# Optimization experiments

Measured on AMD Instinct MI355X. Metric: run time of the kernel, lower is better.

## Reference

```python
import jax, jax.numpy as jnp
import numpy as np

B, N, E = 128, 16384, 1048576
H, C = 512, 10


def setup_inputs() -> dict:
    key = jax.random.key(0)
    ks = jax.random.split(key, 10)
    x = jax.random.normal(ks[0], (B, N), dtype=jnp.float32)
    edge_index = jax.random.randint(ks[1], (2, E), 0, N, dtype=jnp.int64)
    edge_weight = jax.random.uniform(ks[2], (E,), dtype=jnp.float32)
    W1 = jax.random.normal(ks[3], (H, N), dtype=jnp.float32) * (1.0 / np.sqrt(N))
    b1 = jax.random.normal(ks[4], (H,), dtype=jnp.float32) * 0.01
    W2 = jax.random.normal(ks[5], (H, H), dtype=jnp.float32) * (1.0 / np.sqrt(H))
    b2 = jax.random.normal(ks[6], (H,), dtype=jnp.float32) * 0.01
    Wfc = jax.random.normal(ks[7], (C, H), dtype=jnp.float32) * (1.0 / np.sqrt(H))
    bfc = jax.random.normal(ks[8], (C,), dtype=jnp.float32) * 0.01
    return {"x": x, "edge_index": edge_index, "edge_weight": edge_weight,
            "W1": W1, "b1": b1, "W2": W2, "b2": b2, "Wfc": Wfc, "bfc": bfc}


def _sgconv_propagate(x, edge_index, edge_weight):
    """One GCN-normalized propagation (SGConv K=1, lin.weight==1, no bias).
    Batched edge offsets in the original == same operator applied per row.
    x: (B, N); edge_index: (2, E); edge_weight: (E,). Returns (B, N).
    """
    n = x.shape[1]
    src, dst = edge_index[0], edge_index[1]
    loop = jnp.arange(n, dtype=src.dtype)
    src_f = jnp.concatenate([src, loop])
    dst_f = jnp.concatenate([dst, loop])
    w_f = jnp.concatenate([edge_weight, jnp.ones((n,), x.dtype)])  # self-loop weight 1
    deg = jax.ops.segment_sum(w_f, dst_f, num_segments=n)  # in-degree (col)
    dinv = jnp.where(deg > 0, jax.lax.rsqrt(jnp.maximum(deg, 1e-12)), 0.0)
    norm = dinv[src_f] * w_f * dinv[dst_f]  # (E+N,)
    msgs = x[:, src_f] * norm  # (B, E+N) gather + scale
    return jax.ops.segment_sum(msgs.T, dst_f, num_segments=n).T  # scatter-add -> (B, N)


def reference(x, edge_index, edge_weight, W1, b1, W2, b2, Wfc, bfc):
    h = _sgconv_propagate(x, edge_index, edge_weight)  # diffusion (B, N)
    h = jax.nn.relu(h @ W1.T + b1)  # Linear(N->H) + ReLU
    h = jax.nn.relu(h @ W2.T + b2)  # Linear(H->H) + ReLU
    return h @ Wfc.T + bfc  # fc (H->C), softmax=False, dropout=0 (eval)
```

## Files before the change

kernel.cpp:

```cpp
#include <hip/hip_runtime.h>
#include <hip/hip_bf16.h>
#include <stdint.h>

#define B_DIM 128
#define N_DIM 16384
#define E_DIM 1048576
#define H_DIM 512
#define C_DIM 10
#define NWG 256
#define CHUNK (E_DIM / NWG)
#define NWORD8 (N_DIM / 4)
#define NGRP 8
#define WPG (NWG / NGRP)
#define SPLITK 64
#define KC (N_DIM / SPLITK)
#define WMASK 0xFFFFC000u
#define SMASK 0x3FFFu

typedef __attribute__((ext_vector_type(8))) short short8;
typedef __attribute__((ext_vector_type(4))) float f32x4;

__device__ __forceinline__ uint32_t f2bf(float f) {
    uint32_t u = __float_as_uint(f);
    return (u + 0x7fffu + ((u >> 16) & 1u)) >> 16;
}

__device__ __forceinline__ uint32_t encE(int s, float w) {
    uint32_t wb = __float_as_uint(w);
    return ((wb + 0x2000u) & WMASK) | (uint32_t)s;
}

__global__ void __launch_bounds__(256) k_hist1(const int* __restrict__ dst,
                                               uint32_t* __restrict__ slab) {
    __shared__ uint32_t ls[NWORD8];
    int bid = blockIdx.x, t = threadIdx.x;
#pragma unroll
    for (int i = 0; i < NWORD8 / 256; i++) ls[i * 256 + t] = 0;
    __syncthreads();
#pragma unroll
    for (int i = 0; i < CHUNK / 1024; i++) {
        int4 d4 = *(const int4*)&dst[bid * CHUNK + i * 1024 + t * 4];
        atomicAdd(&ls[d4.x >> 2], 1u << ((d4.x & 3) << 3));
        atomicAdd(&ls[d4.y >> 2], 1u << ((d4.y & 3) << 3));
        atomicAdd(&ls[d4.z >> 2], 1u << ((d4.z & 3) << 3));
        atomicAdd(&ls[d4.w >> 2], 1u << ((d4.w & 3) << 3));
    }
    __syncthreads();
#pragma unroll
    for (int i = 0; i < NWORD8 / 256; i++)
        slab[(size_t)bid * NWORD8 + i * 256 + t] = ls[i * 256 + t];
}

__global__ void __launch_bounds__(128) k_scanA8(uint32_t* __restrict__ slab,
                                                uint32_t* __restrict__ grp) {
    int b = blockIdx.x;
    int g = b >> 5;
    int j = (b & 31) * 128 + threadIdx.x;
    uint32_t run = 0;
    for (int w = g * WPG; w < (g + 1) * WPG; w++) {
        uint32_t c = slab[(size_t)w * NWORD8 + j];
        slab[(size_t)w * NWORD8 + j] = run;
        run += c;
    }
    grp[(size_t)g * NWORD8 + j] = run;
}

__global__ void __launch_bounds__(1024) k_scanBC8(uint32_t* __restrict__ grp,
                                                  int* __restrict__ offs) {
    __shared__ uint32_t part[1024];
    int t = threadIdx.x;
    uint32_t tw[4];
    int loc[16];
    uint32_t s = 0;
    int k = 0;
#pragma unroll
    for (int i = 0; i < 4; i++) {
        int j = t * 4 + i;
        uint32_t run = 0;
#pragma unroll
        for (int g = 0; g < NGRP; g++) {
            uint32_t c = grp[(size_t)g * NWORD8 + j];
            grp[(size_t)g * NWORD8 + j] = run;
            run += c;
        }
        tw[i] = run;
#pragma unroll
        for (int b4 = 0; b4 < 4; b4++) {
            loc[k] = (int)s;
            s += (tw[i] >> (b4 * 8)) & 0xffu;
            k++;
        }
    }
    part[t] = s;
    __syncthreads();
    for (int off = 1; off < 1024; off <<= 1) {
        uint32_t v = (t >= off) ? part[t - off] : 0;
        __syncthreads();
        part[t] += v;
        __syncthreads();
    }
    uint32_t ex = (t == 0) ? 0 : part[t - 1];
#pragma unroll
    for (int i = 0; i < 16; i++) offs[t * 16 + i] = (int)(ex + loc[i]);
    if (t == 1023) offs[N_DIM] = (int)part[1023];
}

__global__ void __launch_bounds__(256) k_place2(const int* __restrict__ src,
                                                const int* __restrict__ dst,
                                                const float* __restrict__ ew,
                                                const uint32_t* __restrict__ slab,
                                                const uint32_t* __restrict__ grp,
                                                const int* __restrict__ offs,
                                                uint32_t* __restrict__ packed) {
    __shared__ uint32_t cur[N_DIM];
    int w = blockIdx.x, t = threadIdx.x;
    int g = w >> 5;
#pragma unroll
    for (int i = 0; i < NWORD8 / 256; i++) {
        int j = i * 256 + t;
        uint32_t pv = slab[(size_t)w * NWORD8 + j];
        uint32_t gv = grp[(size_t)g * NWORD8 + j];
        int4 o = *(const int4*)&offs[4 * j];
        cur[4 * j + 0] = (uint32_t)o.x + (gv & 0xffu) + (pv & 0xffu);
        cur[4 * j + 1] = (uint32_t)o.y + ((gv >> 8) & 0xffu) + ((pv >> 8) & 0xffu);
        cur[4 * j + 2] = (uint32_t)o.z + ((gv >> 16) & 0xffu) + ((pv >> 16) & 0xffu);
        cur[4 * j + 3] = (uint32_t)o.w + (gv >> 24) + (pv >> 24);
    }
    __syncthreads();
#pragma unroll
    for (int i = 0; i < CHUNK / 1024; i++) {
        int e = w * CHUNK + i * 1024 + t * 4;
        int4 s4 = *(const int4*)&src[e];
        int4 d4 = *(const int4*)&dst[e];
        float4 w4 = *(const float4*)&ew[e];
        uint32_t p0 = atomicAdd(&cur[d4.x], 1u);
        packed[p0] = encE(s4.x, w4.x);
        uint32_t p1 = atomicAdd(&cur[d4.y], 1u);
        packed[p1] = encE(s4.y, w4.y);
        uint32_t p2 = atomicAdd(&cur[d4.z], 1u);
        packed[p2] = encE(s4.z, w4.z);
        uint32_t p3 = atomicAdd(&cur[d4.w], 1u);
        packed[p3] = encE(s4.w, w4.w);
    }
}

__global__ void __launch_bounds__(256) k_degscale(const int* __restrict__ offs,
                                                  const uint32_t* __restrict__ packed,
                                                  const float* __restrict__ x,
                                                  float* __restrict__ dinv,
                                                  uint16_t* __restrict__ xTh) {
    __shared__ float tile[16][132];
    __shared__ float dvs[16];
    int bid = blockIdx.x;
    int d0 = bid * 16;
    int t = threadIdx.x;
    int wave = t >> 6, lane = t & 63;
#pragma unroll
    for (int i = 0; i < 4; i++) {
        int dl = wave * 4 + i;
        int d = d0 + dl;
        int e0 = offs[d], e1 = offs[d + 1];
        float s = 0.f;
        for (int e = e0 + lane; e < e1; e += 64)
            s += __uint_as_float(packed[e] & WMASK);
#pragma unroll
        for (int o = 32; o > 0; o >>= 1) s += __shfl_down(s, o);
        if (lane == 0) {
            float dv = rsqrtf(s + 1.0f);
            dvs[dl] = dv;
            dinv[d] = dv;
        }
    }
    int dl = t & 15, bg = t >> 4;
#pragma unroll
    for (int i = 0; i < 8; i++) {
        int b = bg * 8 + i;
        tile[dl][b] = x[(size_t)b * N_DIM + d0 + dl];
    }
    __syncthreads();
    int r = t >> 4, cg = t & 15;
    float dv = dvs[r];
    uint4 w;
    uint32_t* wp = (uint32_t*)&w;
#pragma unroll
    for (int j = 0; j < 4; j++) {
        float a = tile[r][cg * 8 + j * 2] * dv;
        float b = tile[r][cg * 8 + j * 2 + 1] * dv;
        wp[j] = f2bf(a) | (f2bf(b) << 16);
    }
    *(uint4*)&xTh[(size_t)(d0 + r) * B_DIM + cg * 8] = w;
}

__global__ void __launch_bounds__(256) k_diffuse(const uint16_t* __restrict__ xTh,
                                                 const int* __restrict__ offs,
                                                 const uint32_t* __restrict__ packed,
                                                 const float* __restrict__ dinv,
                                                 uint16_t* __restrict__ hB) {
    __shared__ uint4 ls[128];
    int wave = threadIdx.x >> 6;
    int d0 = blockIdx.x * 8 + wave * 2;
    int lane = threadIdx.x & 63;
    int g = lane >> 4;
    int colh = lane & 15;
    const uint4* x4 = (const uint4*)xTh;
    int oA = offs[d0], oM = offs[d0 + 1], oB = offs[d0 + 2];
    int eA = oA + lane;
    uint32_t pA = (eA < oM) ? packed[eA] : 0u;
    int eB = oM + lane;
    uint32_t pB = (eB < oB) ? packed[eB] : 0u;
    float accA[8], accB[8];
#pragma unroll
    for (int k = 0; k < 8; k++) { accA[k] = 0.f; accB[k] = 0.f; }
    for (int base = oA; base < oM; base += 64) {
        uint32_t pc = pA;
        int en = base + 64 + lane;
        pA = (en < oM) ? packed[en] : 0u;
#pragma unroll
        for (int i = 0; i < 64; i += 4) {
            uint32_t ev = (uint32_t)__shfl((int)pc, i + g);
            int sx = (int)(ev & SMASK);
            float nm = __uint_as_float(ev & WMASK);
            uint4 xs = x4[(size_t)sx * 16 + colh];
            accA[0] = fmaf(nm, __uint_as_float(xs.x << 16), accA[0]);
            accA[1] = fmaf(nm, __uint_as_float(xs.x & 0xffff0000u), accA[1]);
            accA[2] = fmaf(nm, __uint_as_float(xs.y << 16), accA[2]);
            accA[3] = fmaf(nm, __uint_as_float(xs.y & 0xffff0000u), accA[3]);
            accA[4] = fmaf(nm, __uint_as_float(xs.z << 16), accA[4]);
            accA[5] = fmaf(nm, __uint_as_float(xs.z & 0xffff0000u), accA[5]);
            accA[6] = fmaf(nm, __uint_as_float(xs.w << 16), accA[6]);
            accA[7] = fmaf(nm, __uint_as_float(xs.w & 0xffff0000u), accA[7]);
        }
    }
    for (int base = oM; base < oB; base += 64) {
        uint32_t pc = pB;
        int en = base + 64 + lane;
        pB = (en < oB) ? packed[en] : 0u;
#pragma unroll
        for (int i = 0; i < 64; i += 4) {
            uint32_t ev = (uint32_t)__shfl((int)pc, i + g);
            int sx = (int)(ev & SMASK);
            float nm = __uint_as_float(ev & WMASK);
            uint4 xs = x4[(size_t)sx * 16 + colh];
            accB[0] = fmaf(nm, __uint_as_float(xs.x << 16), accB[0]);
            accB[1] = fmaf(nm, __uint_as_float(xs.x & 0xffff0000u), accB[1]);
            accB[2] = fmaf(nm, __uint_as_float(xs.y << 16), accB[2]);
            accB[3] = fmaf(nm, __uint_as_float(xs.y & 0xffff0000u), accB[3]);
            accB[4] = fmaf(nm, __uint_as_float(xs.z << 16), accB[4]);
            accB[5] = fmaf(nm, __uint_as_float(xs.z & 0xffff0000u), accB[5]);
            accB[6] = fmaf(nm, __uint_as_float(xs.w << 16), accB[6]);
            accB[7] = fmaf(nm, __uint_as_float(xs.w & 0xffff0000u), accB[7]);
        }
    }
#pragma unroll
    for (int off = 16; off <= 32; off <<= 1)
#pragma unroll
        for (int k = 0; k < 8; k++) {
            accA[k] += __shfl_xor(accA[k], off);
            accB[k] += __shfl_xor(accB[k], off);
        }
    int who = lane >> 4;
    if (who < 2) {
        int dd = d0 + who;
        float dv = dinv[dd];
        uint4 sv = x4[(size_t)dd * 16 + colh];
        float o[8];
#pragma unroll
        for (int k = 0; k < 8; k++) o[k] = (who == 0) ? accA[k] : accB[k];
        o[0] = (o[0] + __uint_as_float(sv.x << 16)) * dv;
        o[1] = (o[1] + __uint_as_float(sv.x & 0xffff0000u)) * dv;
        o[2] = (o[2] + __uint_as_float(sv.y << 16)) * dv;
        o[3] = (o[3] + __uint_as_float(sv.y & 0xffff0000u)) * dv;
        o[4] = (o[4] + __uint_as_float(sv.z << 16)) * dv;
        o[5] = (o[5] + __uint_as_float(sv.z & 0xffff0000u)) * dv;
        o[6] = (o[6] + __uint_as_float(sv.w << 16)) * dv;
        o[7] = (o[7] + __uint_as_float(sv.w & 0xffff0000u)) * dv;
        uint4 r;
        r.x = f2bf(o[0]) | (f2bf(o[1]) << 16);
        r.y = f2bf(o[2]) | (f2bf(o[3]) << 16);
        r.z = f2bf(o[4]) | (f2bf(o[5]) << 16);
        r.w = f2bf(o[6]) | (f2bf(o[7]) << 16);
        ls[(wave * 2 + who) * 16 + colh] = r;
    }
    __syncthreads();
    int t = threadIdx.x;
    if (t < 128) {
        const uint16_t* l16 = (const uint16_t*)ls;
        uint16_t v0 = l16[0 * 128 + t], v1 = l16[1 * 128 + t];
        uint16_t v2 = l16[2 * 128 + t], v3 = l16[3 * 128 + t];
        uint16_t v4 = l16[4 * 128 + t], v5 = l16[5 * 128 + t];
        uint16_t v6 = l16[6 * 128 + t], v7 = l16[7 * 128 + t];
        uint4 r;
        r.x = (uint32_t)v0 | ((uint32_t)v1 << 16);
        r.y = (uint32_t)v2 | ((uint32_t)v3 << 16);
        r.z = (uint32_t)v4 | ((uint32_t)v5 << 16);
        r.w = (uint32_t)v6 | ((uint32_t)v7 << 16);
        *(uint4*)&hB[(size_t)t * N_DIM + blockIdx.x * 8] = r;
    }
}

__global__ void __launch_bounds__(256) k_gemm1(const float* __restrict__ W1,
                                               const uint16_t* __restrict__ hB,
                                               float* __restrict__ part) {
    int kc = blockIdx.x;
    int mt = blockIdx.y;
    int t = threadIdx.x, w = t >> 6, l = t & 63;
    int lr = l & 15;
    int lk = (l >> 4) * 8;
    int row = mt * 64 + w * 16 + lr;
    int k0 = kc * KC;
    f32x4 acc[8] = {};
    const float* wbase = W1 + (size_t)row * N_DIM + k0 + lk;
    const uint16_t* hbase = hB + k0 + lk;
#pragma unroll 2
    for (int ks = 0; ks < KC; ks += 32) {
        float4 wa = *(const float4*)(wbase + ks);
        float4 wb = *(const float4*)(wbase + ks + 4);
        short8 bf[8];
#pragma unroll
        for (int c = 0; c < 8; c++)
            bf[c] = *(const short8*)(hbase + (size_t)(c * 16 + lr) * N_DIM + ks);
        float wv0 = wa.x, wv1 = wa.y, wv2 = wa.z, wv3 = wa.w;
        float wv4 = wb.x, wv5 = wb.y, wv6 = wb.z, wv7 = wb.w;
        short8 ahi, alo;
        uint32_t h0;
        h0 = f2bf(wv0); ahi[0] = (short)h0; alo[0] = (short)f2bf(wv0 - __uint_as_float(h0 << 16));
        h0 = f2bf(wv1); ahi[1] = (short)h0; alo[1] = (short)f2bf(wv1 - __uint_as_float(h0 << 16));
        h0 = f2bf(wv2); ahi[2] = (short)h0; alo[2] = (short)f2bf(wv2 - __uint_as_float(h0 << 16));
        h0 = f2bf(wv3); ahi[3] = (short)h0; alo[3] = (short)f2bf(wv3 - __uint_as_float(h0 << 16));
        h0 = f2bf(wv4); ahi[4] = (short)h0; alo[4] = (short)f2bf(wv4 - __uint_as_float(h0 << 16));
        h0 = f2bf(wv5); ahi[5] = (short)h0; alo[5] = (short)f2bf(wv5 - __uint_as_float(h0 << 16));
        h0 = f2bf(wv6); ahi[6] = (short)h0; alo[6] = (short)f2bf(wv6 - __uint_as_float(h0 << 16));
        h0 = f2bf(wv7); ahi[7] = (short)h0; alo[7] = (short)f2bf(wv7 - __uint_as_float(h0 << 16));
#pragma unroll
        for (int c = 0; c < 8; c++) {
            acc[c] = __builtin_amdgcn_mfma_f32_16x16x32_bf16(ahi, bf[c], acc[c], 0, 0, 0);
            acc[c] = __builtin_amdgcn_mfma_f32_16x16x32_bf16(alo, bf[c], acc[c], 0, 0, 0);
        }
    }
    float* pbase = part + (size_t)kc * (H_DIM * B_DIM);
    int j0 = mt * 64 + w * 16 + (l >> 4) * 4;
#pragma unroll
    for (int c = 0; c < 8; c++) {
        int b = c * 16 + lr;
        *(f32x4*)&pbase[(size_t)b * H_DIM + j0] = acc[c];
    }
}

__global__ void __launch_bounds__(1024) k_tail123(const float* __restrict__ part,
                                                  const float* __restrict__ b1,
                                                  const float* __restrict__ W2,
                                                  const float* __restrict__ b2,
                                                  const float* __restrict__ Wfc,
                                                  const float* __restrict__ bfc,
                                                  float* __restrict__ out) {
    __shared__ float h1s[H_DIM];
    __shared__ float h2s[H_DIM];
    int b = blockIdx.x;
    int t = threadIdx.x;
    {
        int j = t & 511, half = t >> 9;
        const float* pb = part + (size_t)b * H_DIM + j
                        + (size_t)half * (SPLITK / 2) * (H_DIM * B_DIM);
        float acc = 0.f;
#pragma unroll
        for (int c = 0; c < SPLITK / 2; c++)
            acc += pb[(size_t)c * (H_DIM * B_DIM)];
        if (half == 0) h1s[j] = acc;
        __syncthreads();
        if (half == 1) h1s[j] = fmaxf(h1s[j] + acc + b1[j], 0.f);
        __syncthreads();
    }
    int w = t >> 6;
    int l = t & 63;
    float hv[8];
#pragma unroll
    for (int k = 0; k < 8; k++) hv[k] = h1s[k * 64 + l];
#pragma unroll
    for (int it = 0; it < 4; it++) {
        int j0 = w * 32 + it * 8;
        float outv = 0.f;
#pragma unroll
        for (int jj = 0; jj < 8; jj++) {
            const float* wrow = W2 + (size_t)(j0 + jj) * H_DIM;
            float a = 0.f;
#pragma unroll
            for (int k = 0; k < 8; k++) a = fmaf(wrow[k * 64 + l], hv[k], a);
#pragma unroll
            for (int o = 1; o < 64; o <<= 1) a += __shfl_xor(a, o);
            if (l == jj) outv = a;
        }
        if (l < 8) h2s[j0 + l] = fmaxf(outv + b2[j0 + l], 0.f);
    }
    __syncthreads();
    if (w == 0) {
        float hv2[8];
#pragma unroll
        for (int k = 0; k < 8; k++) hv2[k] = h2s[k * 64 + l];
        float outv = 0.f;
#pragma unroll
        for (int c = 0; c < C_DIM; c++) {
            const float* wrow = Wfc + (size_t)c * H_DIM;
            float a = 0.f;
#pragma unroll
            for (int k = 0; k < 8; k++) a = fmaf(wrow[k * 64 + l], hv2[k], a);
#pragma unroll
            for (int o = 1; o < 64; o <<= 1) a += __shfl_xor(a, o);
            if (l == c) outv = a;
        }
        if (l < C_DIM) out[b * C_DIM + l] = outv + bfc[l];
    }
}

extern "C" void kernel_launch(void* const* d_in, const int* in_sizes, int n_in,
                              void* d_out, int out_size, void* d_ws, size_t ws_size,
                              hipStream_t stream) {
    const float* x   = (const float*)d_in[0];
    const int*   ei  = (const int*)d_in[1];
    const float* ew  = (const float*)d_in[2];
    const float* W1  = (const float*)d_in[3];
    const float* b1  = (const float*)d_in[4];
    const float* W2  = (const float*)d_in[5];
    const float* b2  = (const float*)d_in[6];
    const float* Wfc = (const float*)d_in[7];
    const float* bfc = (const float*)d_in[8];
    float* out = (float*)d_out;

    const int* src = ei;
    const int* dst = ei + E_DIM;

    char* ws = (char*)d_ws;
    size_t off = 0;
    auto alloc = [&](size_t bytes) -> void* {
        void* p = ws + off;
        off = (off + bytes + 255) & ~(size_t)255;
        return p;
    };
    uint16_t* xTh   = (uint16_t*)alloc((size_t)N_DIM * B_DIM * 2);
    uint32_t* packed = (uint32_t*)alloc((size_t)E_DIM * 4);
    size_t sort_bytes = (size_t)NWG * NWORD8 * 4 + (size_t)NGRP * NWORD8 * 4;
    size_t part_bytes = (size_t)SPLITK * H_DIM * B_DIM * 4;
    char* scratch = (char*)alloc(sort_bytes > part_bytes ? sort_bytes : part_bytes);
    int*   offs   = (int*)  alloc((size_t)(N_DIM + 1) * 4);
    float* dinv   = (float*)alloc((size_t)N_DIM * 4);
    uint16_t* hB  = (uint16_t*)alloc((size_t)B_DIM * N_DIM * 2);
    uint32_t* slab = (uint32_t*)scratch;
    uint32_t* grp  = (uint32_t*)(scratch + (size_t)NWG * NWORD8 * 4);
    float* part    = (float*)scratch;
    if (off > ws_size) return;

    k_hist1<<<NWG, 256, 0, stream>>>(dst, slab);
    k_scanA8<<<NWG, 128, 0, stream>>>(slab, grp);
    k_scanBC8<<<1, 1024, 0, stream>>>(grp, offs);
    k_place2<<<NWG, 256, 0, stream>>>(src, dst, ew, slab, grp, offs, packed);
    k_degscale<<<N_DIM / 16, 256, 0, stream>>>(offs, packed, x, dinv, xTh);
    k_diffuse<<<N_DIM / 8, 256, 0, stream>>>(xTh, offs, packed, dinv, hB);
    k_gemm1<<<dim3(SPLITK, H_DIM / 64), 256, 0, stream>>>(W1, hB, part);
    k_tail123<<<B_DIM, 1024, 0, stream>>>(part, b1, W2, b2, Wfc, bfc, out);
}
```

Before: 115.7 us.

## Fuse scan kernels via last-block atomic counter and halve GEMM split-K

Merges the two scan stages into one launch: 32 blocks of 1024 threads each do per-group column scans, and the last block to finish (found with an atomic counter reset in the histogram kernel) does the global scan into offsets. This removes one kernel launch and its inter-kernel gap. It also halves SPLITK for the first GEMM, giving fewer partial buffers to reduce but fewer workgroups. The first scan stage now runs on 32 workgroups instead of 256, which lowers its parallelism.

```diff
diff --git a/kernel.cpp b/kernel.cpp
--- a/kernel.cpp
+++ b/kernel.cpp
@@ -12,7 +12,7 @@
 #define NWORD8 (N_DIM / 4)
 #define NGRP 8
 #define WPG (NWG / NGRP)
-#define SPLITK 64
+#define SPLITK 32
 #define KC (N_DIM / SPLITK)
 #define WMASK 0xFFFFC000u
 #define SMASK 0x3FFFu
@@ -31,9 +31,11 @@
 }
 
 __global__ void __launch_bounds__(256) k_hist1(const int* __restrict__ dst,
-                                               uint32_t* __restrict__ slab) {
+                                               uint32_t* __restrict__ slab,
+                                               int* __restrict__ done) {
     __shared__ uint32_t ls[NWORD8];
     int bid = blockIdx.x, t = threadIdx.x;
+    if (bid == 0 && t == 0) *done = 0;
 #pragma unroll
     for (int i = 0; i < NWORD8 / 256; i++) ls[i * 256 + t] = 0;
     __syncthreads();
@@ -51,36 +53,45 @@
         slab[(size_t)bid * NWORD8 + i * 256 + t] = ls[i * 256 + t];
 }
 
-__global__ void __launch_bounds__(128) k_scanA8(uint32_t* __restrict__ slab,
-                                                uint32_t* __restrict__ grp) {
+__global__ void __launch_bounds__(1024) k_scanAB(uint32_t* __restrict__ slab,
+                                                 uint32_t* __restrict__ grp,
+                                                 int* __restrict__ offs,
+                                                 int* __restrict__ done) {
+    __shared__ uint32_t part[1024];
+    __shared__ int amLast;
     int b = blockIdx.x;
-    int g = b >> 5;
-    int j = (b & 31) * 128 + threadIdx.x;
-    uint32_t run = 0;
-    for (int w = g * WPG; w < (g + 1) * WPG; w++) {
-        uint32_t c = slab[(size_t)w * NWORD8 + j];
-        slab[(size_t)w * NWORD8 + j] = run;
-        run += c;
-    }
-    grp[(size_t)g * NWORD8 + j] = run;
-}
-
-__global__ void __launch_bounds__(1024) k_scanBC8(uint32_t* __restrict__ grp,
-                                                  int* __restrict__ offs) {
-    __shared__ uint32_t part[1024];
     int t = threadIdx.x;
+    int g = b >> 2;
+    int j = (b & 3) * 1024 + t;
+    {
+        uint32_t run = 0;
+        for (int w = g * WPG; w < (g + 1) * WPG; w++) {
+            uint32_t c = slab[(size_t)w * NWORD8 + j];
+            slab[(size_t)w * NWORD8 + j] = run;
+            run += c;
+        }
+        grp[(size_t)g * NWORD8 + j] = run;
+    }
+    __syncthreads();
+    if (t == 0) {
+        __threadfence();
+        amLast = (atomicAdd(done, 1) == 31);
+    }
+    __syncthreads();
+    if (!amLast) return;
+    __threadfence();
     uint32_t tw[4];
     int loc[16];
     uint32_t s = 0;
     int k = 0;
 #pragma unroll
     for (int i = 0; i < 4; i++) {
-        int j = t * 4 + i;
+        int jj = t * 4 + i;
         uint32_t run = 0;
 #pragma unroll
-        for (int g = 0; g < NGRP; g++) {
-            uint32_t c = grp[(size_t)g * NWORD8 + j];
-            grp[(size_t)g * NWORD8 + j] = run;
+        for (int gg = 0; gg < NGRP; gg++) {
+            uint32_t c = grp[(size_t)gg * NWORD8 + jj];
+            grp[(size_t)gg * NWORD8 + jj] = run;
             run += c;
         }
         tw[i] = run;
@@ -443,14 +454,14 @@
     int*   offs   = (int*)  alloc((size_t)(N_DIM + 1) * 4);
     float* dinv   = (float*)alloc((size_t)N_DIM * 4);
     uint16_t* hB  = (uint16_t*)alloc((size_t)B_DIM * N_DIM * 2);
+    int*   done   = (int*)  alloc(256);
     uint32_t* slab = (uint32_t*)scratch;
     uint32_t* grp  = (uint32_t*)(scratch + (size_t)NWG * NWORD8 * 4);
     float* part    = (float*)scratch;
     if (off > ws_size) return;
 
-    k_hist1<<<NWG, 256, 0, stream>>>(dst, slab);
-    k_scanA8<<<NWG, 128, 0, stream>>>(slab, grp);
-    k_scanBC8<<<1, 1024, 0, stream>>>(grp, offs);
+    k_hist1<<<NWG, 256, 0, stream>>>(dst, slab, done);
+    k_scanAB<<<32, 1024, 0, stream>>>(slab, grp, offs, done);
     k_place2<<<NWG, 256, 0, stream>>>(src, dst, ew, slab, grp, offs, packed);
     k_degscale<<<N_DIM / 16, 256, 0, stream>>>(offs, packed, x, dinv, xTh);
     k_diffuse<<<N_DIM / 8, 256, 0, stream>>>(xTh, offs, packed, dinv, hB);
```

After: 118.2 us. 1.02x slower.
